# Kernel tuning notes

Measured on AMD Instinct MI355X. Metric: run time of the kernel, lower is better.

Reference implementation:

```python
import jax, jax.numpy as jnp
import numpy as np

B, S, H, F = 16, 2048, 1024, 1024


def sparsemax(z, axis):
    # standard sparsemax (Martins & Astudillo 2016) along `axis`
    z_sorted = -jnp.sort(-z, axis=axis)
    K = z.shape[axis]
    shp = [1] * z.ndim
    shp[axis] = K
    k = jnp.arange(1, K + 1, dtype=z.dtype).reshape(shp)
    cum = jnp.cumsum(z_sorted, axis=axis)
    support = (1.0 + k * z_sorted) > cum
    k_sel = jnp.sum(support, axis=axis, keepdims=True)
    cum_sel = jnp.take_along_axis(cum, k_sel.astype(jnp.int32) - 1, axis=axis)
    tau = (cum_sel - 1.0) / k_sel.astype(z.dtype)
    return jnp.maximum(z - tau, 0.0)


def additive_attention(query, values, w1, w2, attn_bias, v):
    # query: [B,F,1] -> permuted to [B,1,F]; values: [B,S,F]
    q = jnp.swapaxes(query, -2, -1)  # [B,1,F]
    t1 = q @ w1 + values @ w2        # [B,S,F] (broadcast over S)
    energy = jnp.tanh(t1 + attn_bias)
    return energy @ v                # [B,S,1]


def setup_inputs() -> dict:
    key = jax.random.key(0)
    ks = jax.random.split(key, 12)
    s = 0.02
    return {
        "attention_mask": jnp.ones((B, S), jnp.float32),
        "xlnet_output": jax.random.normal(ks[0], (B, S, H), jnp.float32),
        "item_weights": jax.random.uniform(ks[1], (B, S, 1), jnp.float32),
        "W_C": jax.random.normal(ks[2], (H, F), jnp.float32) * s,
        "b_C": jnp.zeros((F,), jnp.float32),
        "W_A": jax.random.normal(ks[3], (H, F), jnp.float32) * s,
        "b_A": jnp.zeros((F,), jnp.float32),
        "w1": jax.random.normal(ks[4], (F, F), jnp.float32) * s,
        "w2": jax.random.normal(ks[5], (F, F), jnp.float32) * s,
        "attn_bias": jnp.zeros((1, 1, F), jnp.float32),
        "v": jax.random.normal(ks[6], (F, 1), jnp.float32) * s,
        "w_1": jnp.ones((1,), jnp.float32),
        "w_2": jnp.ones((1,), jnp.float32),
        "w_3": jnp.ones((1,), jnp.float32),
        "layer_i": 0,
        "proactive_masking": 0,
    }


def reference(attention_mask, xlnet_output, item_weights, W_C, b_C, W_A, b_A,
              w1, w2, attn_bias, v, w_1, w_2, w_3, layer_i, proactive_masking):
    # attend-to-real-token mask: (1-m)*-10000 -> [B,S,1]
    mask_add = ((1.0 - attention_mask) * -10000.0)[..., None]
    # projections + ReLU (dropout in eval mode = identity; proactive_masking=0)
    C = jax.nn.relu(xlnet_output @ W_C + b_C)  # [B,S,F]
    A = jax.nn.relu(xlnet_output @ W_A + b_A)  # [B,S,F]
    # q = C^T @ item_weights -> [B,F,1]
    q = jnp.einsum('bsf,bso->bfo', C, item_weights)
    alpha = additive_attention(q, C, w1, w2, attn_bias, v) + mask_add
    alpha = jax.nn.softmax(alpha, axis=1)        # [B,S,1]
    h = jnp.einsum('bsf,bso->bfo', C, alpha)     # [B,F,1]
    L = additive_attention(h, A, w1, w2, attn_bias, v)  # [B,S,1]
    if layer_i == 0:
        x = w_3 ** 2 - w_2 ** 2 - w_1 ** 2
    elif layer_i == 1:
        x = w_3 ** 2 - w_2 ** 2
    else:
        x = w_3 ** 2
    L = L * jax.nn.sigmoid(x)
    L = L + mask_add
    L = sparsemax(L, axis=1)
    return (h, L, A)
```

## Files before the change

kernel.cpp:

```cpp
#include <hip/hip_runtime.h>
#include <hip/hip_bf16.h>
#include <math.h>

typedef __hip_bfloat16 bf16;
typedef __bf16 bf16x8 __attribute__((ext_vector_type(8)));
typedef float f32x4 __attribute__((ext_vector_type(4)));

#define BDIM 16
#define SDIM 2048
#define FDIM 1024
#define BS (BDIM * SDIM)

__device__ __forceinline__ float bf2f(bf16 x) { return __bfloat162float(x); }
__device__ __forceinline__ bf16 f2bf(float x) { return __float2bfloat16(x); }

__device__ __forceinline__ void gload16(const void* g, void* l) {
  __builtin_amdgcn_global_load_lds(
      (const __attribute__((address_space(1))) unsigned int*)g,
      (__attribute__((address_space(3))) unsigned int*)l, 16, 0, 0);
}

template <int MODE, int OUTK>
__global__ __launch_bounds__(256) void gemm_glds(
    const bf16* __restrict__ Ag, const bf16* __restrict__ Bg,
    const float* __restrict__ bias, bf16* __restrict__ outb,
    float* __restrict__ outf, const float* __restrict__ t1,
    const float* __restrict__ vvec, float* __restrict__ logit) {
  constexpr int BK = 32, K = 1024;
  __shared__ __align__(16) bf16 As[128 * BK];
  __shared__ __align__(16) bf16 Bs[128 * BK];

  const int tid = threadIdx.x;
  const int lane = tid & 63;
  const int wave = tid >> 6;
  const int wm = (wave & 1) * 64;
  const int wn = (wave >> 1) * 64;
  const int tile_m = blockIdx.x * 128;
  const int tile_n = blockIdx.y * 128;
  const int ln = lane & 15;
  const int ko = (lane >> 4) * 8;

  f32x4 acc[4][4] = {};

  const int lrow = wave * 16 + (lane >> 2);
  const int lcolb = (lane & 3) * 16;
  const char* gA0 = (const char*)(Ag + (size_t)(tile_m + lrow) * K) + lcolb;
  const char* gA1 = (const char*)(Ag + (size_t)(tile_m + lrow + 64) * K) + lcolb;
  const char* gB0 = (const char*)(Bg + (size_t)(tile_n + lrow) * K) + lcolb;
  const char* gB1 = (const char*)(Bg + (size_t)(tile_n + lrow + 64) * K) + lcolb;
  char* lA0 = (char*)As + wave * 1024;
  char* lA1 = lA0 + 4096;
  char* lB0 = (char*)Bs + wave * 1024;
  char* lB1 = lB0 + 4096;

  for (int k0 = 0; k0 < K; k0 += BK) {
    __syncthreads();
    gload16(gA0, lA0);
    gload16(gA1, lA1);
    gload16(gB0, lB0);
    gload16(gB1, lB1);
    gA0 += 64; gA1 += 64; gB0 += 64; gB1 += 64;
    __syncthreads();
    bf16x8 af[4], bfr[4];
#pragma unroll
    for (int i = 0; i < 4; i++)
      af[i] = *(const bf16x8*)&As[(wm + i * 16 + ln) * BK + ko];
#pragma unroll
    for (int j = 0; j < 4; j++)
      bfr[j] = *(const bf16x8*)&Bs[(wn + j * 16 + ln) * BK + ko];
#pragma unroll
    for (int i = 0; i < 4; i++)
#pragma unroll
      for (int j = 0; j < 4; j++)
        acc[i][j] =
            __builtin_amdgcn_mfma_f32_16x16x32_bf16(af[i], bfr[j], acc[i][j], 0, 0, 0);
  }

  if (MODE == 0) {
#pragma unroll
    for (int i = 0; i < 4; i++) {
#pragma unroll
      for (int j = 0; j < 4; j++) {
        const int colg = tile_n + wn + j * 16 + ln;
        const float bv = bias[colg];
#pragma unroll
        for (int r = 0; r < 4; r++) {
          const int rowg = tile_m + wm + i * 16 + ((lane >> 4) << 2) + r;
          const float val = fmaxf(acc[i][j][r] + bv, 0.f);
          if constexpr (OUTK != 1) outb[(size_t)rowg * FDIM + colg] = f2bf(val);
          if constexpr (OUTK != 0) outf[(size_t)rowg * FDIM + colg] = val;
        }
      }
    }
  } else {
    const int b = tile_m >> 11;
    float tcol[4], vcol[4];
#pragma unroll
    for (int j = 0; j < 4; j++) {
      const int colg = tile_n + wn + j * 16 + ln;
      tcol[j] = t1[b * FDIM + colg];
      vcol[j] = vvec[colg];
    }
#pragma unroll
    for (int i = 0; i < 4; i++) {
#pragma unroll
      for (int r = 0; r < 4; r++) {
        float s = 0.f;
#pragma unroll
        for (int j = 0; j < 4; j++) s += tanhf(acc[i][j][r] + tcol[j]) * vcol[j];
        s += __shfl_xor(s, 1);
        s += __shfl_xor(s, 2);
        s += __shfl_xor(s, 4);
        s += __shfl_xor(s, 8);
        if (ln == 0) {
          const int rowg = tile_m + wm + i * 16 + ((lane >> 4) << 2) + r;
          atomicAdd(&logit[rowg], s);
        }
      }
    }
  }
}

template <int MODE, bool AF32, bool OUTF32>
__global__ __launch_bounds__(256) void gemm_bt(
    const void* __restrict__ Agv, const bf16* __restrict__ Bg,
    const float* __restrict__ bias, void* __restrict__ outp,
    const float* __restrict__ t1, const float* __restrict__ vvec,
    float* __restrict__ logit) {
  constexpr int BK = 32, K = 1024, LDP = 56;
  __shared__ __align__(16) bf16 As[128 * LDP];
  __shared__ __align__(16) bf16 Bs[128 * LDP];

  const int tid = threadIdx.x;
  const int lane = tid & 63;
  const int wave = tid >> 6;
  const int wm = (wave & 1) * 64;
  const int wn = (wave >> 1) * 64;
  const int tile_m = blockIdx.x * 128;
  const int tile_n = blockIdx.y * 128;
  const int ln = lane & 15;
  const int ko = (lane >> 4) * 8;

  f32x4 acc[4][4] = {};

  const int arow = tid >> 2;
  const int acol = (tid & 3) * 8;
  const size_t aoff = (size_t)(tile_m + arow) * K + acol;
  const size_t aoff2 = aoff + (size_t)64 * K;
  const bf16* gB = Bg + (size_t)(tile_n + arow) * K + acol;
  const size_t rstep = (size_t)64 * K;
  bf16* lA = &As[arow * LDP + acol];
  bf16* lA2 = &As[(64 + arow) * LDP + acol];
  bf16* lB = &Bs[arow * LDP + acol];
  bf16* lB2 = &Bs[(64 + arow) * LDP + acol];

  for (int k0 = 0; k0 < K; k0 += BK) {
    bf16x8 va, va2;
    if constexpr (AF32) {
      const float* pa = (const float*)Agv + aoff + k0;
      const float* pa2 = (const float*)Agv + aoff2 + k0;
      const float4 x0 = *(const float4*)pa, x1 = *(const float4*)(pa + 4);
      const float4 y0 = *(const float4*)pa2, y1 = *(const float4*)(pa2 + 4);
      va[0] = (__bf16)x0.x; va[1] = (__bf16)x0.y; va[2] = (__bf16)x0.z; va[3] = (__bf16)x0.w;
      va[4] = (__bf16)x1.x; va[5] = (__bf16)x1.y; va[6] = (__bf16)x1.z; va[7] = (__bf16)x1.w;
      va2[0] = (__bf16)y0.x; va2[1] = (__bf16)y0.y; va2[2] = (__bf16)y0.z; va2[3] = (__bf16)y0.w;
      va2[4] = (__bf16)y1.x; va2[5] = (__bf16)y1.y; va2[6] = (__bf16)y1.z; va2[7] = (__bf16)y1.w;
    } else {
      va = *(const bf16x8*)((const bf16*)Agv + aoff + k0);
      va2 = *(const bf16x8*)((const bf16*)Agv + aoff2 + k0);
    }
    const bf16x8 vb = *(const bf16x8*)(gB + k0);
    const bf16x8 vb2 = *(const bf16x8*)(gB + k0 + rstep);
    __syncthreads();
    *(bf16x8*)lA = va;
    *(bf16x8*)lA2 = va2;
    *(bf16x8*)lB = vb;
    *(bf16x8*)lB2 = vb2;
    __syncthreads();
    bf16x8 af[4], bfr[4];
#pragma unroll
    for (int i = 0; i < 4; i++)
      af[i] = *(const bf16x8*)&As[(wm + i * 16 + ln) * LDP + ko];
#pragma unroll
    for (int j = 0; j < 4; j++)
      bfr[j] = *(const bf16x8*)&Bs[(wn + j * 16 + ln) * LDP + ko];
#pragma unroll
    for (int i = 0; i < 4; i++)
#pragma unroll
      for (int j = 0; j < 4; j++)
        acc[i][j] =
            __builtin_amdgcn_mfma_f32_16x16x32_bf16(af[i], bfr[j], acc[i][j], 0, 0, 0);
  }

  if (MODE == 0) {
#pragma unroll
    for (int i = 0; i < 4; i++) {
#pragma unroll
      for (int j = 0; j < 4; j++) {
        const int colg = tile_n + wn + j * 16 + ln;
        const float bv = bias[colg];
#pragma unroll
        for (int r = 0; r < 4; r++) {
          const int rowg = tile_m + wm + i * 16 + ((lane >> 4) << 2) + r;
          const float val = fmaxf(acc[i][j][r] + bv, 0.f);
          if constexpr (OUTF32)
            ((float*)outp)[(size_t)rowg * FDIM + colg] = val;
          else
            ((bf16*)outp)[(size_t)rowg * FDIM + colg] = f2bf(val);
        }
      }
    }
  } else {
    const int b = tile_m >> 11;
    float tcol[4], vcol[4];
#pragma unroll
    for (int j = 0; j < 4; j++) {
      const int colg = tile_n + wn + j * 16 + ln;
      tcol[j] = t1[b * FDIM + colg];
      vcol[j] = vvec[colg];
    }
#pragma unroll
    for (int i = 0; i < 4; i++) {
#pragma unroll
      for (int r = 0; r < 4; r++) {
        float s = 0.f;
#pragma unroll
        for (int j = 0; j < 4; j++) s += tanhf(acc[i][j][r] + tcol[j]) * vcol[j];
        s += __shfl_xor(s, 1);
        s += __shfl_xor(s, 2);
        s += __shfl_xor(s, 4);
        s += __shfl_xor(s, 8);
        if (ln == 0) {
          const int rowg = tile_m + wm + i * 16 + ((lane >> 4) << 2) + r;
          atomicAdd(&logit[rowg], s);
        }
      }
    }
  }
}

__global__ void transpose_cvt_k(const float* __restrict__ src, bf16* __restrict__ dst,
                                int K, int N) {
  __shared__ bf16 t[32][33];
  const int n0 = blockIdx.x * 32, k0 = blockIdx.y * 32;
  const int tx = threadIdx.x, ty = threadIdx.y;
  for (int i = 0; i < 32; i += 8)
    t[ty + i][tx] = f2bf(src[(size_t)(k0 + ty + i) * N + n0 + tx]);
  __syncthreads();
  for (int i = 0; i < 32; i += 8)
    dst[(size_t)(n0 + ty + i) * K + k0 + tx] = t[tx][ty + i];
}

__global__ void cvt_bf16_k(const float* __restrict__ in, bf16* __restrict__ out) {
  const size_t i = ((size_t)blockIdx.x * 256 + threadIdx.x) * 8;
  const float4 a = *(const float4*)(in + i);
  const float4 b = *(const float4*)(in + i + 4);
  bf16x8 o;
  o[0] = (__bf16)a.x; o[1] = (__bf16)a.y; o[2] = (__bf16)a.z; o[3] = (__bf16)a.w;
  o[4] = (__bf16)b.x; o[5] = (__bf16)b.y; o[6] = (__bf16)b.z; o[7] = (__bf16)b.w;
  *(bf16x8*)(out + i) = o;
}

__global__ void zerof_k(float* __restrict__ a, int n) {
  const int i = blockIdx.x * 256 + threadIdx.x;
  if (i < n) a[i] = 0.f;
}

__global__ void copyf_k(const float* __restrict__ in, float* __restrict__ out, int n) {
  const int i = blockIdx.x * 256 + threadIdx.x;
  if (i < n) out[i] = in[i];
}

__global__ void colreduce_k(const bf16* __restrict__ M, const float* __restrict__ w,
                            float* __restrict__ outf) {
  const int b = blockIdx.y;
  const int f = blockIdx.x * 256 + threadIdx.x;
  const int s0 = blockIdx.z * 128;
  const bf16* col = M + ((size_t)b * SDIM + s0) * FDIM + f;
  const float* wb = w + b * SDIM + s0;
  float acc = 0.f;
#pragma unroll 8
  for (int s = 0; s < 128; ++s) acc += bf2f(col[(size_t)s * FDIM]) * wb[s];
  atomicAdd(&outf[b * FDIM + f], acc);
}

__global__ void smallgemm_k(const float* __restrict__ invec, const float* __restrict__ w1,
                            const float* __restrict__ bias, float* __restrict__ out) {
  const int b = blockIdx.y;
  const int n = blockIdx.x * 256 + threadIdx.x;
  const float* q = invec + b * FDIM;
  float acc = 0.f;
#pragma unroll 8
  for (int f = 0; f < FDIM; ++f) acc += q[f] * w1[(size_t)f * FDIM + n];
  out[b * FDIM + n] = acc + bias[n];
}

__global__ void softmax_k(const float* __restrict__ logit, const float* __restrict__ mask,
                          float* __restrict__ alpha) {
  const int b = blockIdx.x, tid = threadIdx.x;
  __shared__ float red[4];
  float v[8];
  float lmax = -1e30f;
#pragma unroll
  for (int k = 0; k < 8; ++k) {
    const int s = tid + k * 256;
    const float m = (1.f - mask[b * SDIM + s]) * -10000.f;
    v[k] = logit[b * SDIM + s] + m;
    lmax = fmaxf(lmax, v[k]);
  }
  for (int m = 1; m < 64; m <<= 1) lmax = fmaxf(lmax, __shfl_xor(lmax, m));
  if ((tid & 63) == 0) red[tid >> 6] = lmax;
  __syncthreads();
  lmax = fmaxf(fmaxf(red[0], red[1]), fmaxf(red[2], red[3]));
  __syncthreads();
  float lsum = 0.f;
#pragma unroll
  for (int k = 0; k < 8; ++k) {
    v[k] = expf(v[k] - lmax);
    lsum += v[k];
  }
  for (int m = 1; m < 64; m <<= 1) lsum += __shfl_xor(lsum, m);
  if ((tid & 63) == 0) red[tid >> 6] = lsum;
  __syncthreads();
  const float inv = 1.f / (red[0] + red[1] + red[2] + red[3]);
#pragma unroll
  for (int k = 0; k < 8; ++k) alpha[b * SDIM + tid + k * 256] = v[k] * inv;
}

__global__ void sparsemax_k(const float* __restrict__ Ll, const float* __restrict__ mask,
                            const float* __restrict__ w1s, const float* __restrict__ w2s,
                            const float* __restrict__ w3s, const int* __restrict__ layer_i,
                            float* __restrict__ Lout) {
  const int b = blockIdx.x, tid = threadIdx.x;
  __shared__ float red[4];
  const float a1 = w1s[0], a2 = w2s[0], a3 = w3s[0];
  const int li = layer_i[0];
  const float x = (li == 0) ? (a3 * a3 - a2 * a2 - a1 * a1)
                            : ((li == 1) ? (a3 * a3 - a2 * a2) : (a3 * a3));
  const float sig = 1.f / (1.f + expf(-x));
  float z[8];
  float lmax = -1e30f;
#pragma unroll
  for (int k = 0; k < 8; ++k) {
    const int s = tid + k * 256;
    const float m = (1.f - mask[b * SDIM + s]) * -10000.f;
    z[k] = Ll[b * SDIM + s] * sig + m;
    lmax = fmaxf(lmax, z[k]);
  }
  for (int m = 1; m < 64; m <<= 1) lmax = fmaxf(lmax, __shfl_xor(lmax, m));
  if ((tid & 63) == 0) red[tid >> 6] = lmax;
  __syncthreads();
  const float zmax = fmaxf(fmaxf(red[0], red[1]), fmaxf(red[2], red[3]));
  __syncthreads();
  float lo = zmax - 1.f, hi = zmax;
  for (int it = 0; it < 40; ++it) {
    const float tau = 0.5f * (lo + hi);
    float ssum = 0.f;
#pragma unroll
    for (int k = 0; k < 8; ++k) ssum += fmaxf(z[k] - tau, 0.f);
    for (int m = 1; m < 64; m <<= 1) ssum += __shfl_xor(ssum, m);
    if ((tid & 63) == 0) red[tid >> 6] = ssum;
    __syncthreads();
    const float tot = red[0] + red[1] + red[2] + red[3];
    __syncthreads();
    if (tot > 1.f) lo = tau; else hi = tau;
  }
  const float tau = 0.5f * (lo + hi);
#pragma unroll
  for (int k = 0; k < 8; ++k)
    Lout[b * SDIM + tid + k * 256] = fmaxf(z[k] - tau, 0.f);
}

extern "C" void kernel_launch(void* const* d_in, const int* in_sizes, int n_in,
                              void* d_out, int out_size, void* d_ws, size_t ws_size,
                              hipStream_t stream) {
  const float* mask = (const float*)d_in[0];
  const float* xlnet = (const float*)d_in[1];
  const float* iw = (const float*)d_in[2];
  const float* W_C = (const float*)d_in[3];
  const float* b_C = (const float*)d_in[4];
  const float* W_A = (const float*)d_in[5];
  const float* b_A = (const float*)d_in[6];
  const float* w1 = (const float*)d_in[7];
  const float* w2 = (const float*)d_in[8];
  const float* attn_bias = (const float*)d_in[9];
  const float* v = (const float*)d_in[10];
  const float* w_1 = (const float*)d_in[11];
  const float* w_2 = (const float*)d_in[12];
  const float* w_3 = (const float*)d_in[13];
  const int* layer_i = (const int*)d_in[14];

  float* out = (float*)d_out;
  float* h_out = out;
  float* L_out = out + 16384;
  float* A_out = out + 49152;
  bf16* Cbuf = (bf16*)A_out;

  char* ws = (char*)d_ws;
  bf16* WT_C = (bf16*)(ws);
  bf16* WT_A = (bf16*)(ws + 2097152);
  bf16* w2T = (bf16*)(ws + 4194304);
  float* qbuf = (float*)(ws + 6291456);
  float* t1q = (float*)(ws + 6356992);
  float* t1h = (float*)(ws + 6422528);
  float* hbuf = (float*)(ws + 6488064);
  float* a_logit = (float*)(ws + 6553600);
  float* alpha = (float*)(ws + 6684672);
  float* L_logit = (float*)(ws + 6815744);
  bf16* Xbf = (bf16*)(ws + 6946816);
  bf16* Abf = (bf16*)(ws + 74055680);
  const bool t1ok = ws_size >= (size_t)74055680;
  const bool t2ok = ws_size >= (size_t)141164544;

  const dim3 tb(32, 8);
  transpose_cvt_k<<<dim3(32, 32), tb, 0, stream>>>(W_C, WT_C, 1024, 1024);
  transpose_cvt_k<<<dim3(32, 32), tb, 0, stream>>>(W_A, WT_A, 1024, 1024);
  transpose_cvt_k<<<dim3(32, 32), tb, 0, stream>>>(w2, w2T, 1024, 1024);
  zerof_k<<<640, 256, 0, stream>>>(qbuf, 163840);

  const dim3 gg(BS / 128, FDIM / 128);

  if (t1ok)
    cvt_bf16_k<<<16384, 256, 0, stream>>>(xlnet, Xbf);

  if (t1ok)
    gemm_glds<0, 0><<<gg, 256, 0, stream>>>(Xbf, WT_C, b_C, Cbuf, nullptr,
                                            nullptr, nullptr, nullptr);
  else
    gemm_bt<0, true, false><<<gg, 256, 0, stream>>>(xlnet, WT_C, b_C, Cbuf,
                                                    nullptr, nullptr, nullptr);
  colreduce_k<<<dim3(4, BDIM, 16), 256, 0, stream>>>(Cbuf, iw, qbuf);
  smallgemm_k<<<dim3(4, BDIM), 256, 0, stream>>>(qbuf, w1, attn_bias, t1q);
  if (t1ok)
    gemm_glds<1, 0><<<gg, 256, 0, stream>>>(Cbuf, w2T, nullptr, nullptr,
                                            nullptr, t1q, v, a_logit);
  else
    gemm_bt<1, false, false><<<gg, 256, 0, stream>>>(Cbuf, w2T, nullptr,
                                                     nullptr, t1q, v, a_logit);
  softmax_k<<<BDIM, 256, 0, stream>>>(a_logit, mask, alpha);
  colreduce_k<<<dim3(4, BDIM, 16), 256, 0, stream>>>(Cbuf, alpha, hbuf);
  copyf_k<<<64, 256, 0, stream>>>(hbuf, h_out, BDIM * FDIM);
  smallgemm_k<<<dim3(4, BDIM), 256, 0, stream>>>(hbuf, w1, attn_bias, t1h);

  if (t2ok)
    gemm_glds<0, 2><<<gg, 256, 0, stream>>>(Xbf, WT_A, b_A, Abf, A_out,
                                            nullptr, nullptr, nullptr);
  else if (t1ok)
    gemm_glds<0, 1><<<gg, 256, 0, stream>>>(Xbf, WT_A, b_A, nullptr, A_out,
                                            nullptr, nullptr, nullptr);
  else
    gemm_bt<0, true, true><<<gg, 256, 0, stream>>>(xlnet, WT_A, b_A, A_out,
                                                   nullptr, nullptr, nullptr);
  if (t2ok)
    gemm_glds<1, 0><<<gg, 256, 0, stream>>>(Abf, w2T, nullptr, nullptr,
                                            nullptr, t1h, v, L_logit);
  else
    gemm_bt<1, true, false><<<gg, 256, 0, stream>>>(A_out, w2T, nullptr,
                                                    nullptr, t1h, v, L_logit);
  sparsemax_k<<<BDIM, 256, 0, stream>>>(L_logit, mask, w_1, w_2, w_3, layer_i, L_out);
}
```

Baseline: 828.5 us.

## Fuse C and A projection GEMMs sharing X tiles; dual-tile energy GEMMs

Adds a gemm_dual kernel that, in mode 0, computes both the C and A projections from one shared load of each X tile, writing C into a new workspace buffer and A in both fp32 and bf16. In mode 1 each block reuses one w2T tile across two 128-row tiles of C or A, halving the weight-tile reloads in the tanh-energy GEMMs. The three weight transposes are merged into one launch. This trades more LDS and accumulator registers per block, and a larger workspace requirement, for fewer global reads and fewer kernel launches. Mode 1 is now launched without the workspace-size fallback for the first energy GEMM.

```diff
diff --git a/kernel.cpp b/kernel.cpp
--- a/kernel.cpp
+++ b/kernel.cpp
@@ -18,6 +18,140 @@
   __builtin_amdgcn_global_load_lds(
       (const __attribute__((address_space(1))) unsigned int*)g,
       (__attribute__((address_space(3))) unsigned int*)l, 16, 0, 0);
+}
+
+template <int MODE>
+__global__ __launch_bounds__(512, 4) void gemm_dual(
+    const bf16* __restrict__ Sg, const bf16* __restrict__ T0g,
+    const bf16* __restrict__ T1g, const float* __restrict__ bias0,
+    const float* __restrict__ bias1, bf16* __restrict__ out0b,
+    bf16* __restrict__ out1b, float* __restrict__ out1f,
+    const float* __restrict__ t1, const float* __restrict__ vvec,
+    float* __restrict__ logit) {
+  constexpr int BK = 32, K = 1024;
+  __shared__ __align__(16) bf16 Ss[128 * BK];
+  __shared__ __align__(16) bf16 T0s[128 * BK];
+  __shared__ __align__(16) bf16 T1s[128 * BK];
+
+  const int tid = threadIdx.x;
+  const int lane = tid & 63;
+  const int wave = tid >> 6;
+  const int wm = (wave & 1) * 64;
+  const int wn = (wave >> 1) * 32;
+  const int ln = lane & 15;
+  const int ko = (lane >> 4) * 8;
+
+  const int srow0 = (MODE == 0) ? blockIdx.x * 128 : blockIdx.y * 128;
+  const int t0row0 = (MODE == 0) ? blockIdx.y * 128 : blockIdx.x * 256;
+  const int t1row0 = t0row0 + ((MODE == 0) ? 0 : 128);
+
+  f32x4 acc0[4][2] = {};
+  f32x4 acc1[4][2] = {};
+
+  const int lrow = wave * 16 + (lane >> 2);
+  const int lcolb = (lane & 3) * 16;
+  const char* gS = (const char*)(Sg + (size_t)(srow0 + lrow) * K) + lcolb;
+  const char* gT0 = (const char*)(T0g + (size_t)(t0row0 + lrow) * K) + lcolb;
+  const char* gT1 = (const char*)(T1g + (size_t)(t1row0 + lrow) * K) + lcolb;
+  char* lS = (char*)Ss + wave * 1024;
+  char* lT0 = (char*)T0s + wave * 1024;
+  char* lT1 = (char*)T1s + wave * 1024;
+
+  for (int k0 = 0; k0 < K; k0 += BK) {
+    __syncthreads();
+    gload16(gS, lS);
+    gload16(gT0, lT0);
+    gload16(gT1, lT1);
+    gS += 64; gT0 += 64; gT1 += 64;
+    __syncthreads();
+    if constexpr (MODE == 0) {
+      bf16x8 av[4], b0[2], b1[2];
+#pragma unroll
+      for (int i = 0; i < 4; i++)
+        av[i] = *(const bf16x8*)&Ss[(wm + i * 16 + ln) * BK + ko];
+#pragma unroll
+      for (int j = 0; j < 2; j++) {
+        b0[j] = *(const bf16x8*)&T0s[(wn + j * 16 + ln) * BK + ko];
+        b1[j] = *(const bf16x8*)&T1s[(wn + j * 16 + ln) * BK + ko];
+      }
+#pragma unroll
+      for (int i = 0; i < 4; i++)
+#pragma unroll
+        for (int j = 0; j < 2; j++) {
+          acc0[i][j] = __builtin_amdgcn_mfma_f32_16x16x32_bf16(av[i], b0[j], acc0[i][j], 0, 0, 0);
+          acc1[i][j] = __builtin_amdgcn_mfma_f32_16x16x32_bf16(av[i], b1[j], acc1[i][j], 0, 0, 0);
+        }
+    } else {
+      bf16x8 bv[2], a0[4], a1[4];
+#pragma unroll
+      for (int j = 0; j < 2; j++)
+        bv[j] = *(const bf16x8*)&Ss[(wn + j * 16 + ln) * BK + ko];
+#pragma unroll
+      for (int i = 0; i < 4; i++) {
+        a0[i] = *(const bf16x8*)&T0s[(wm + i * 16 + ln) * BK + ko];
+        a1[i] = *(const bf16x8*)&T1s[(wm + i * 16 + ln) * BK + ko];
+      }
+#pragma unroll
+      for (int i = 0; i < 4; i++)
+#pragma unroll
+        for (int j = 0; j < 2; j++) {
+          acc0[i][j] = __builtin_amdgcn_mfma_f32_16x16x32_bf16(a0[i], bv[j], acc0[i][j], 0, 0, 0);
+          acc1[i][j] = __builtin_amdgcn_mfma_f32_16x16x32_bf16(a1[i], bv[j], acc1[i][j], 0, 0, 0);
+        }
+    }
+  }
+
+  const int q4 = (lane >> 4) << 2;
+  if constexpr (MODE == 0) {
+#pragma unroll
+    for (int i = 0; i < 4; i++) {
+#pragma unroll
+      for (int j = 0; j < 2; j++) {
+        const int colg = blockIdx.y * 128 + wn + j * 16 + ln;
+        const float bC = bias0[colg];
+        const float bA = bias1[colg];
+#pragma unroll
+        for (int r = 0; r < 4; r++) {
+          const int rowg = blockIdx.x * 128 + wm + i * 16 + q4 + r;
+          const float c = fmaxf(acc0[i][j][r] + bC, 0.f);
+          const float a = fmaxf(acc1[i][j][r] + bA, 0.f);
+          out0b[(size_t)rowg * FDIM + colg] = f2bf(c);
+          out1f[(size_t)rowg * FDIM + colg] = a;
+          out1b[(size_t)rowg * FDIM + colg] = f2bf(a);
+        }
+      }
+    }
+  } else {
+    const int b = t0row0 >> 11;
+    float tcol[2], vcol[2];
+#pragma unroll
+    for (int j = 0; j < 2; j++) {
+      const int colg = blockIdx.y * 128 + wn + j * 16 + ln;
+      tcol[j] = t1[b * FDIM + colg];
+      vcol[j] = vvec[colg];
+    }
+#pragma unroll
+    for (int t = 0; t < 2; t++) {
+#pragma unroll
+      for (int i = 0; i < 4; i++) {
+#pragma unroll
+        for (int r = 0; r < 4; r++) {
+          float s = 0.f;
+#pragma unroll
+          for (int j = 0; j < 2; j++)
+            s += tanhf((t ? acc1[i][j][r] : acc0[i][j][r]) + tcol[j]) * vcol[j];
+          s += __shfl_xor(s, 1);
+          s += __shfl_xor(s, 2);
+          s += __shfl_xor(s, 4);
+          s += __shfl_xor(s, 8);
+          if (ln == 0) {
+            const int rowg = (t ? t1row0 : t0row0) + wm + i * 16 + q4 + r;
+            atomicAdd(&logit[rowg], s);
+          }
+        }
+      }
+    }
+  }
 }
 
 template <int MODE, int OUTK>
@@ -239,16 +373,19 @@
   }
 }
 
-__global__ void transpose_cvt_k(const float* __restrict__ src, bf16* __restrict__ dst,
-                                int K, int N) {
+__global__ void transpose_cvt3_k(const float* __restrict__ s0, const float* __restrict__ s1,
+                                 const float* __restrict__ s2, bf16* __restrict__ d0,
+                                 bf16* __restrict__ d1, bf16* __restrict__ d2) {
   __shared__ bf16 t[32][33];
+  const float* src = (blockIdx.z == 0) ? s0 : (blockIdx.z == 1) ? s1 : s2;
+  bf16* dst = (blockIdx.z == 0) ? d0 : (blockIdx.z == 1) ? d1 : d2;
   const int n0 = blockIdx.x * 32, k0 = blockIdx.y * 32;
   const int tx = threadIdx.x, ty = threadIdx.y;
   for (int i = 0; i < 32; i += 8)
-    t[ty + i][tx] = f2bf(src[(size_t)(k0 + ty + i) * N + n0 + tx]);
+    t[ty + i][tx] = f2bf(src[(size_t)(k0 + ty + i) * 1024 + n0 + tx]);
   __syncthreads();
   for (int i = 0; i < 32; i += 8)
-    dst[(size_t)(n0 + ty + i) * K + k0 + tx] = t[tx][ty + i];
+    dst[(size_t)(n0 + ty + i) * 1024 + k0 + tx] = t[tx][ty + i];
 }
 
 __global__ void cvt_bf16_k(const float* __restrict__ in, bf16* __restrict__ out) {
@@ -394,7 +531,6 @@
   float* h_out = out;
   float* L_out = out + 16384;
   float* A_out = out + 49152;
-  bf16* Cbuf = (bf16*)A_out;
 
   char* ws = (char*)d_ws;
   bf16* WT_C = (bf16*)(ws);
@@ -409,21 +545,27 @@
   float* L_logit = (float*)(ws + 6815744);
   bf16* Xbf = (bf16*)(ws + 6946816);
   bf16* Abf = (bf16*)(ws + 74055680);
+  bf16* Cws = (bf16*)(ws + 141164544);
   const bool t1ok = ws_size >= (size_t)74055680;
   const bool t2ok = ws_size >= (size_t)141164544;
+  const bool t3ok = ws_size >= (size_t)208273408;
+
+  bf16* Cbuf = t3ok ? Cws : (bf16*)A_out;
 
   const dim3 tb(32, 8);
-  transpose_cvt_k<<<dim3(32, 32), tb, 0, stream>>>(W_C, WT_C, 1024, 1024);
-  transpose_cvt_k<<<dim3(32, 32), tb, 0, stream>>>(W_A, WT_A, 1024, 1024);
-  transpose_cvt_k<<<dim3(32, 32), tb, 0, stream>>>(w2, w2T, 1024, 1024);
+  transpose_cvt3_k<<<dim3(32, 32, 3), tb, 0, stream>>>(W_C, W_A, w2, WT_C, WT_A, w2T);
   zerof_k<<<640, 256, 0, stream>>>(qbuf, 163840);
 
   const dim3 gg(BS / 128, FDIM / 128);
+  const dim3 gd(BS / 256, FDIM / 128);
 
   if (t1ok)
     cvt_bf16_k<<<16384, 256, 0, stream>>>(xlnet, Xbf);
 
-  if (t1ok)
+  if (t3ok)
+    gemm_dual<0><<<gg, 512, 0, stream>>>(Xbf, WT_C, WT_A, b_C, b_A,
+                                         Cbuf, Abf, A_out, nullptr, nullptr, nullptr);
+  else if (t1ok)
     gemm_glds<0, 0><<<gg, 256, 0, stream>>>(Xbf, WT_C, b_C, Cbuf, nullptr,
                                             nullptr, nullptr, nullptr);
   else
@@ -431,29 +573,27 @@
                                                     nullptr, nullptr, nullptr);
   colreduce_k<<<dim3(4, BDIM, 16), 256, 0, stream>>>(Cbuf, iw, qbuf);
   smallgemm_k<<<dim3(4, BDIM), 256, 0, stream>>>(qbuf, w1, attn_bias, t1q);
-  if (t1ok)
-    gemm_glds<1, 0><<<gg, 256, 0, stream>>>(Cbuf, w2T, nullptr, nullptr,
-                                            nullptr, t1q, v, a_logit);
-  else
-    gemm_bt<1, false, false><<<gg, 256, 0, stream>>>(Cbuf, w2T, nullptr,
-                                                     nullptr, t1q, v, a_logit);
+  gemm_dual<1><<<gd, 512, 0, stream>>>(w2T, Cbuf, Cbuf, nullptr, nullptr,
+                                       nullptr, nullptr, nullptr, t1q, v, a_logit);
   softmax_k<<<BDIM, 256, 0, stream>>>(a_logit, mask, alpha);
   colreduce_k<<<dim3(4, BDIM, 16), 256, 0, stream>>>(Cbuf, alpha, hbuf);
   copyf_k<<<64, 256, 0, stream>>>(hbuf, h_out, BDIM * FDIM);
   smallgemm_k<<<dim3(4, BDIM), 256, 0, stream>>>(hbuf, w1, attn_bias, t1h);
 
+  if (!t3ok) {
+    if (t2ok)
+      gemm_glds<0, 2><<<gg, 256, 0, stream>>>(Xbf, WT_A, b_A, Abf, A_out,
+                                              nullptr, nullptr, nullptr);
+    else if (t1ok)
+      gemm_glds<0, 1><<<gg, 256, 0, stream>>>(Xbf, WT_A, b_A, nullptr, A_out,
+                                              nullptr, nullptr, nullptr);
+    else
+      gemm_bt<0, true, true><<<gg, 256, 0, stream>>>(xlnet, WT_A, b_A, A_out,
+                                                     nullptr, nullptr, nullptr);
+  }
   if (t2ok)
-    gemm_glds<0, 2><<<gg, 256, 0, stream>>>(Xbf, WT_A, b_A, Abf, A_out,
-                                            nullptr, nullptr, nullptr);
-  else if (t1ok)
-    gemm_glds<0, 1><<<gg, 256, 0, stream>>>(Xbf, WT_A, b_A, nullptr, A_out,
-                                            nullptr, nullptr, nullptr);
-  else
-    gemm_bt<0, true, true><<<gg, 256, 0, stream>>>(xlnet, WT_A, b_A, A_out,
-                                                   nullptr, nullptr, nullptr);
-  if (t2ok)
-    gemm_glds<1, 0><<<gg, 256, 0, stream>>>(Abf, w2T, nullptr, nullptr,
-                                            nullptr, t1h, v, L_logit);
+    gemm_dual<1><<<gd, 512, 0, stream>>>(w2T, Abf, Abf, nullptr, nullptr,
+                                         nullptr, nullptr, nullptr, t1h, v, L_logit);
   else
     gemm_bt<1, true, false><<<gg, 256, 0, stream>>>(A_out, w2T, nullptr,
                                                     nullptr, t1h, v, L_logit);
```

After: 802.3 us. 3.2% less time.
